# Optimization experiments

Hardware: AMD Instinct MI355X
Metric: run time of the kernel (lower is better)

Reference implementation:

```python
import jax, jax.numpy as jnp
import numpy as np

V, E, H = 32000, 512, 512  # output_dim, emb_dim, hid_dim
B, S = 256, 128


def setup_inputs() -> dict:
    key = jax.random.key(0)
    ks = jax.random.split(key, 16)
    d = {
        'input_ids': jax.random.randint(ks[0], (B,), 0, V),
        'encoded': jax.random.normal(ks[1], (B, S, 2 * H), jnp.float32),
        'src': jax.random.randint(ks[2], (B, S), 0, V),
        'prev_state': jax.random.normal(ks[3], (B, H), jnp.float32),
        'weighted': jax.random.normal(ks[4], (B, 2 * H), jnp.float32),
        'order': 1,
        # parameters (PyTorch layouts: Linear weight is (out,in); GRU gates order r,z,n)
        'embed_w': jax.random.normal(ks[5], (V, E), jnp.float32) * 0.02,
        'gru_w_ih': jax.random.normal(ks[6], (3 * H, E + 2 * H), jnp.float32) * 0.02,
        'gru_w_hh': jax.random.normal(ks[7], (3 * H, H), jnp.float32) * 0.02,
        'gru_b_ih': jnp.zeros((3 * H,), jnp.float32),
        'gru_b_hh': jnp.zeros((3 * H,), jnp.float32),
        'Ws_w': jax.random.normal(ks[8], (H, 2 * H), jnp.float32) * 0.02,
        'Ws_b': jnp.zeros((H,), jnp.float32),
        'Wo_w': jax.random.normal(ks[9], (V, H), jnp.float32) * 0.02,
        'Wo_b': jnp.zeros((V,), jnp.float32),
        'Wc_w': jax.random.normal(ks[10], (H, 2 * H), jnp.float32) * 0.02,
        'Wc_b': jnp.zeros((H,), jnp.float32),
    }
    return d


def _forward(input_ids, encoded, src, prev_state, weighted, order,
             embed_w, gru_w_ih, gru_w_hh, gru_b_ih, gru_b_hh,
             Ws_w, Ws_b, Wo_w, Wo_b, Wc_w, Wc_b):
    b, s, _ = encoded.shape
    v = Wo_w.shape[0]
    if order == 0:
        prev_state = encoded[:, -1] @ Ws_w.T + Ws_b           # (B,H)
        weighted = jnp.zeros((b, 2 * gru_w_hh.shape[1]), encoded.dtype)
    # GRU cell, single step (seq_len=1), torch gate order r,z,n
    x = jnp.concatenate([embed_w[input_ids], weighted], axis=-1)  # (B, E+2H)
    gi = x @ gru_w_ih.T + gru_b_ih
    gh = prev_state @ gru_w_hh.T + gru_b_hh
    i_r, i_z, i_n = jnp.split(gi, 3, axis=-1)
    h_r, h_z, h_n = jnp.split(gh, 3, axis=-1)
    r = jax.nn.sigmoid(i_r + h_r)
    z = jax.nn.sigmoid(i_z + h_z)
    n = jnp.tanh(i_n + r * h_n)
    hidden = (1.0 - z) * n + z * prev_state                    # (B,H)

    score_g = hidden @ Wo_w.T + Wo_b                           # (B,V)
    score_c = jnp.tanh(encoded @ Wc_w.T + Wc_b)                # (B,S,H)
    score_c = jnp.einsum('bsh,bh->bs', score_c, hidden)        # (B,S)
    mask = (src == 0).astype(encoded.dtype) * -1000.0
    score_c = jnp.tanh(score_c + mask)

    probs = jax.nn.softmax(jnp.concatenate([score_g, score_c], axis=1), axis=1)
    prob_g = probs[:, :v]
    prob_c = probs[:, v:]                                      # (B,S)

    # vectorized scatter-add replacing the nested python loops
    rows = jnp.arange(b)[:, None]
    prob_c_to_g = jnp.zeros((b, v), probs.dtype).at[rows, src].add(prob_c)
    predicted = (prob_g + prob_c_to_g)[:, None, :]             # (B,1,V)

    eq = (src == input_ids[:, None]).astype(encoded.dtype)     # (B,S)
    idx = eq / jnp.maximum(eq.sum(axis=1, keepdims=True), 1.0)
    attn = prob_c * idx                                        # (B,S)
    weighted_out = jnp.einsum('bs,bsd->bd', attn, encoded)     # (B,2H)
    return predicted, hidden, weighted_out


def reference(input_ids, encoded, src, prev_state, weighted, order,
              embed_w, gru_w_ih, gru_w_hh, gru_b_ih, gru_b_hh,
              Ws_w, Ws_b, Wo_w, Wo_b, Wc_w, Wc_b):
    return _forward(input_ids, encoded, src, prev_state, weighted, order,
                    embed_w, gru_w_ih, gru_w_hh, gru_b_ih, gru_b_hh,
                    Ws_w, Ws_b, Wo_w, Wo_b, Wc_w, Wc_b)
```

## Files before the change

kernel.cpp:

```cpp
#include <hip/hip_runtime.h>
#include <cstdint>
#include <cstddef>

#define B_ 256
#define S_ 128
#define H_ 512
#define E_ 512
#define V_ 32000
#define NBLK_G (V_ / 64)

typedef _Float16 half_t;
typedef _Float16 half8 __attribute__((ext_vector_type(8)));
typedef float floatx4 __attribute__((ext_vector_type(4)));

__device__ __forceinline__ float sigmoidf_(float x) { return 1.0f / (1.0f + __expf(-x)); }
__device__ __forceinline__ float fast_tanh(float x) {
    float e = __expf(2.0f * x);
    return 1.0f - 2.0f / (e + 1.0f);
}

__global__ __launch_bounds__(256)
void prep_kernel(const int* __restrict__ ids, const float* __restrict__ encoded,
                 const float* __restrict__ prev_state, const float* __restrict__ weighted,
                 const int* __restrict__ order_p, const float* __restrict__ embed,
                 const float* __restrict__ Ws_w, const float* __restrict__ Ws_b,
                 float* __restrict__ x, float* __restrict__ prev)
{
    int i = blockIdx.x * 256 + threadIdx.x;
    int b = i >> 11;
    int j = i & 2047;
    int order = order_p[0];
    if (j < 1536) {
        float v;
        if (j < 512) v = embed[(size_t)ids[b] * E_ + j];
        else         v = (order == 0) ? 0.0f : weighted[b * 1024 + (j - 512)];
        x[b * 1536 + j] = v;
    } else {
        int h = j - 1536;
        float v;
        if (order != 0) {
            v = prev_state[b * H_ + h];
        } else {
            const float* e  = encoded + ((size_t)b * S_ + (S_ - 1)) * 1024;
            const float* wr = Ws_w + (size_t)h * 1024;
            float accv = Ws_b[h];
            for (int k = 0; k < 1024; ++k) accv += e[k] * wr[k];
            v = accv;
        }
        prev[b * H_ + h] = v;
    }
}

__global__ __launch_bounds__(256)
void wc_cvt_kernel(const float* __restrict__ Wc, half_t* __restrict__ out)
{
    int i = blockIdx.x * 256 + threadIdx.x;
    int nc = i & 15;
    int kq = (i >> 4) & 3;
    int kt = (i >> 6) & 31;
    int nt = i >> 11;
    int n  = nt * 16 + nc;
    int k0 = kt * 32 + kq * 8;
    const float* p = Wc + (size_t)n * 1024 + k0;
    float4 a = *(const float4*)p;
    float4 b = *(const float4*)(p + 4);
    half8 h;
    h[0] = (half_t)a.x; h[1] = (half_t)a.y; h[2] = (half_t)a.z; h[3] = (half_t)a.w;
    h[4] = (half_t)b.x; h[5] = (half_t)b.y; h[6] = (half_t)b.z; h[7] = (half_t)b.w;
    *(half8*)(out + (size_t)i * 8) = h;
}

template<int BM, int BN, int WAVES_M, int WAVES_N, int EPI>
__global__ __launch_bounds__(256, 2)
void gemm_f16(const float* __restrict__ A, const float* __restrict__ Bw,
              float* __restrict__ C, const float* __restrict__ bias,
              float* __restrict__ aux, int K, int lda, int ldb, int ldc, int nblk)
{
    constexpr int BK = 32;
    constexpr int WM = BM / WAVES_M;
    constexpr int WN = BN / WAVES_N;
    constexpr int FM = WM / 16;
    constexpr int FN = WN / 16;
    constexpr int A_ITEMS = (BM * 4) / 256;
    constexpr int B_ITEMS = (BN * 4) / 256;

    __shared__ half_t As[BM * BK];
    __shared__ half_t Bs[BN * BK];

    const int tid  = threadIdx.x;
    const int wid  = tid >> 6;
    const int lane = tid & 63;
    const int wm   = wid % WAVES_M;
    const int wn   = wid / WAVES_M;
    const int bm0  = blockIdx.y * BM;
    const int bn0  = blockIdx.x * BN;
    const int col  = lane & 15;
    const int quad = lane >> 4;
    const int swz  = (quad ^ (col & 3)) * 8;

    floatx4 acc[FM][FN] = {};

    for (int kt = 0; kt < K; kt += BK) {
        float4 ar[A_ITEMS][2], br[B_ITEMS][2];
#pragma unroll
        for (int i = 0; i < A_ITEMS; ++i) {
            int idx = tid + i * 256, row = idx >> 2, ch = idx & 3;
            const float* p = A + (size_t)(bm0 + row) * lda + kt + ch * 8;
            ar[i][0] = *(const float4*)p; ar[i][1] = *(const float4*)(p + 4);
        }
#pragma unroll
        for (int i = 0; i < B_ITEMS; ++i) {
            int idx = tid + i * 256, row = idx >> 2, ch = idx & 3;
            const float* p = Bw + (size_t)(bn0 + row) * ldb + kt + ch * 8;
            br[i][0] = *(const float4*)p; br[i][1] = *(const float4*)(p + 4);
        }
        __syncthreads();
#pragma unroll
        for (int i = 0; i < A_ITEMS; ++i) {
            int idx = tid + i * 256, row = idx >> 2, ch = idx & 3;
            int pos = (ch ^ (row & 3)) * 8;
            half8 h;
            h[0] = (half_t)ar[i][0].x; h[1] = (half_t)ar[i][0].y;
            h[2] = (half_t)ar[i][0].z; h[3] = (half_t)ar[i][0].w;
            h[4] = (half_t)ar[i][1].x; h[5] = (half_t)ar[i][1].y;
            h[6] = (half_t)ar[i][1].z; h[7] = (half_t)ar[i][1].w;
            *(half8*)(&As[row * BK + pos]) = h;
        }
#pragma unroll
        for (int i = 0; i < B_ITEMS; ++i) {
            int idx = tid + i * 256, row = idx >> 2, ch = idx & 3;
            int pos = (ch ^ (row & 3)) * 8;
            half8 h;
            h[0] = (half_t)br[i][0].x; h[1] = (half_t)br[i][0].y;
            h[2] = (half_t)br[i][0].z; h[3] = (half_t)br[i][0].w;
            h[4] = (half_t)br[i][1].x; h[5] = (half_t)br[i][1].y;
            h[6] = (half_t)br[i][1].z; h[7] = (half_t)br[i][1].w;
            *(half8*)(&Bs[row * BK + pos]) = h;
        }
        __syncthreads();

        half8 af[FM], bf[FN];
#pragma unroll
        for (int fm = 0; fm < FM; ++fm)
            af[fm] = *(const half8*)(&As[(wm * WM + fm * 16 + col) * BK + swz]);
#pragma unroll
        for (int fn = 0; fn < FN; ++fn)
            bf[fn] = *(const half8*)(&Bs[(wn * WN + fn * 16 + col) * BK + swz]);
#pragma unroll
        for (int fm = 0; fm < FM; ++fm)
#pragma unroll
            for (int fn = 0; fn < FN; ++fn)
                acc[fm][fn] = __builtin_amdgcn_mfma_f32_16x16x32_f16(af[fm], bf[fn], acc[fm][fn], 0, 0, 0);
    }

    if constexpr (EPI == 0) {
#pragma unroll
        for (int fm = 0; fm < FM; ++fm) {
            int m0 = bm0 + wm * WM + fm * 16 + quad * 4;
#pragma unroll
            for (int fn = 0; fn < FN; ++fn) {
                int n = bn0 + wn * WN + fn * 16 + col;
                float bv = bias[n];
#pragma unroll
                for (int r = 0; r < 4; ++r)
                    C[(size_t)(m0 + r) * ldc + n] = acc[fm][fn][r] + bv;
            }
        }
    } else {
        const int bx = blockIdx.x;
#pragma unroll
        for (int fm = 0; fm < FM; ++fm) {
            int m0 = bm0 + wm * WM + fm * 16 + quad * 4;
            float vv[FN][4];
#pragma unroll
            for (int fn = 0; fn < FN; ++fn) {
                int n = bn0 + fn * 16 + col;
                float bv = bias[n];
#pragma unroll
                for (int r = 0; r < 4; ++r) {
                    vv[fn][r] = acc[fm][fn][r] + bv;
                    C[(size_t)(m0 + r) * ldc + n] = vv[fn][r];
                }
            }
#pragma unroll
            for (int r = 0; r < 4; ++r) {
                float mx = vv[0][r];
#pragma unroll
                for (int fn = 1; fn < FN; ++fn) mx = fmaxf(mx, vv[fn][r]);
#pragma unroll
                for (int off = 1; off < 16; off <<= 1)
                    mx = fmaxf(mx, __shfl_xor(mx, off, 64));
                float se = 0.f;
#pragma unroll
                for (int fn = 0; fn < FN; ++fn) se += __expf(vv[fn][r] - mx);
#pragma unroll
                for (int off = 1; off < 16; off <<= 1)
                    se += __shfl_xor(se, off, 64);
                if (col == 0) {
                    aux[(size_t)(m0 + r) * nblk + bx] = mx;
                    aux[(size_t)256 * nblk + (size_t)(m0 + r) * nblk + bx] = se;
                }
            }
        }
    }
}

__global__ __launch_bounds__(512, 4)
void wc_sc_kernel(const float* __restrict__ enc, const half_t* __restrict__ WcT,
                  const float* __restrict__ bias, const float* __restrict__ hidden,
                  float* __restrict__ sc_out)
{
    __shared__ half_t As[2][64 * 32];
    __shared__ float  s_part[8 * 64];

    const int tid  = threadIdx.x;
    const int wid  = tid >> 6;
    const int lane = tid & 63;
    const int col  = lane & 15;
    const int quad = lane >> 4;
    const int swz  = (quad ^ (col & 3)) * 8;
    const int bm0  = blockIdx.x * 64;

    const int ar_row = tid >> 2;
    const int ar_ch  = tid & 3;
    const float* aptr = enc + (size_t)(bm0 + ar_row) * 1024 + ar_ch * 8;
    const int a_pos = ar_row * 32 + (ar_ch ^ (ar_row & 3)) * 8;

    const half_t* bq = WcT + (size_t)wid * 4 * 16384 + quad * 128 + col * 8;

    floatx4 acc[4][4] = {};
    float4 ar0, ar1;
    half8 bf0[4], bf1[4];

    if (tid < 256) { ar0 = *(const float4*)(aptr); ar1 = *(const float4*)(aptr + 4); }
#pragma unroll
    for (int fn = 0; fn < 4; ++fn)
        bf0[fn] = *(const half8*)(bq + fn * 16384);

    for (int t2 = 0; t2 < 16; ++t2) {
        const int kA = t2 * 64;
        if (tid < 256) {
            half8 h;
            h[0] = (half_t)ar0.x; h[1] = (half_t)ar0.y; h[2] = (half_t)ar0.z; h[3] = (half_t)ar0.w;
            h[4] = (half_t)ar1.x; h[5] = (half_t)ar1.y; h[6] = (half_t)ar1.z; h[7] = (half_t)ar1.w;
            *(half8*)(&As[0][a_pos]) = h;
        }
        __syncthreads();
        if (tid < 256) {
            ar0 = *(const float4*)(aptr + kA + 32);
            ar1 = *(const float4*)(aptr + kA + 36);
        }
#pragma unroll
        for (int fn = 0; fn < 4; ++fn)
            bf1[fn] = *(const half8*)(bq + fn * 16384 + (2 * t2 + 1) * 512);
#pragma unroll
        for (int fm = 0; fm < 4; ++fm) {
            half8 af = *(const half8*)(&As[0][(fm * 16 + col) * 32 + swz]);
#pragma unroll
            for (int fn = 0; fn < 4; ++fn)
                acc[fm][fn] = __builtin_amdgcn_mfma_f32_16x16x32_f16(af, bf0[fn], acc[fm][fn], 0, 0, 0);
        }
        if (tid < 256) {
            half8 h;
            h[0] = (half_t)ar0.x; h[1] = (half_t)ar0.y; h[2] = (half_t)ar0.z; h[3] = (half_t)ar0.w;
            h[4] = (half_t)ar1.x; h[5] = (half_t)ar1.y; h[6] = (half_t)ar1.z; h[7] = (half_t)ar1.w;
            *(half8*)(&As[1][a_pos]) = h;
        }
        __syncthreads();
        if (t2 < 15) {
            if (tid < 256) {
                ar0 = *(const float4*)(aptr + kA + 64);
                ar1 = *(const float4*)(aptr + kA + 68);
            }
#pragma unroll
            for (int fn = 0; fn < 4; ++fn)
                bf0[fn] = *(const half8*)(bq + fn * 16384 + (2 * t2 + 2) * 512);
        }
#pragma unroll
        for (int fm = 0; fm < 4; ++fm) {
            half8 af = *(const half8*)(&As[1][(fm * 16 + col) * 32 + swz]);
#pragma unroll
            for (int fn = 0; fn < 4; ++fn)
                acc[fm][fn] = __builtin_amdgcn_mfma_f32_16x16x32_f16(af, bf1[fn], acc[fm][fn], 0, 0, 0);
        }
    }

    const float* hid = hidden + (size_t)(bm0 >> 7) * H_;
#pragma unroll
    for (int fm = 0; fm < 4; ++fm) {
        float p0 = 0.f, p1 = 0.f, p2 = 0.f, p3 = 0.f;
#pragma unroll
        for (int fn = 0; fn < 4; ++fn) {
            int n = wid * 64 + fn * 16 + col;
            float bv = bias[n];
            float hv = hid[n];
            p0 += fast_tanh(acc[fm][fn][0] + bv) * hv;
            p1 += fast_tanh(acc[fm][fn][1] + bv) * hv;
            p2 += fast_tanh(acc[fm][fn][2] + bv) * hv;
            p3 += fast_tanh(acc[fm][fn][3] + bv) * hv;
        }
#pragma unroll
        for (int off = 1; off < 16; off <<= 1) {
            p0 += __shfl_xor(p0, off, 64);
            p1 += __shfl_xor(p1, off, 64);
            p2 += __shfl_xor(p2, off, 64);
            p3 += __shfl_xor(p3, off, 64);
        }
        if (col == 0) {
            int rloc = fm * 16 + quad * 4;
            s_part[wid * 64 + rloc + 0] = p0;
            s_part[wid * 64 + rloc + 1] = p1;
            s_part[wid * 64 + rloc + 2] = p2;
            s_part[wid * 64 + rloc + 3] = p3;
        }
    }
    __syncthreads();
    if (tid < 64) {
        float s = 0.f;
#pragma unroll
        for (int w = 0; w < 8; ++w) s += s_part[w * 64 + tid];
        sc_out[bm0 + tid] = s;
    }
}

__global__ __launch_bounds__(256)
void gate_kernel(const float* __restrict__ gi, const float* __restrict__ gh,
                 const float* __restrict__ prev, float* __restrict__ hidden)
{
    int i = blockIdx.x * 256 + threadIdx.x;
    int b = i >> 9;
    int h = i & 511;
    const float* gib = gi + (size_t)b * 1536;
    const float* ghb = gh + (size_t)b * 1536;
    float r = sigmoidf_(gib[h] + ghb[h]);
    float z = sigmoidf_(gib[h + 512] + ghb[h + 512]);
    float n = tanhf(gib[h + 1024] + r * ghb[h + 1024]);
    hidden[i] = (1.0f - z) * n + z * prev[i];
}

__global__ __launch_bounds__(256)
void final_kernel(const float* __restrict__ sc_raw,
                  const int* __restrict__ src, const int* __restrict__ ids,
                  const float* __restrict__ encoded, const float* __restrict__ parts,
                  float* __restrict__ predicted, float* __restrict__ weighted_out)
{
    int b = blockIdx.x;
    int t = threadIdx.x;
    __shared__ float s_scf[S_];
    __shared__ float s_attn[S_];
    __shared__ int   s_src[S_];
    __shared__ float rm[4], rs[4];
    __shared__ int   s_cnt;

    float* pred = predicted + (size_t)b * V_;
    const float* pm = parts + (size_t)b * NBLK_G;
    const float* ps = parts + (size_t)256 * NBLK_G + (size_t)b * NBLK_G;

    if (t < S_) {
        int sv = src[b * S_ + t];
        s_src[t] = sv;
        float raw = sc_raw[b * S_ + t];
        if (sv == 0) raw -= 1000.0f;
        s_scf[t] = tanhf(raw);
    }

    float m = -1e30f, s = 0.f;
    for (int j = t; j < NBLK_G; j += 256) {
        float mo = pm[j], so = ps[j];
        float mn = fmaxf(m, mo);
        s = s * __expf(m - mn) + so * __expf(mo - mn);
        m = mn;
    }
    __syncthreads();
    if (t < S_) {
        float x = s_scf[t];
        float mn = fmaxf(m, x);
        s = s * __expf(m - mn) + __expf(x - mn);
        m = mn;
    }
#pragma unroll
    for (int off = 1; off < 64; off <<= 1) {
        float mo = __shfl_xor(m, off, 64);
        float so = __shfl_xor(s, off, 64);
        float mn = fmaxf(m, mo);
        s = s * __expf(m - mn) + so * __expf(mo - mn);
        m = mn;
    }
    if ((t & 63) == 0) { rm[t >> 6] = m; rs[t >> 6] = s; }
    __syncthreads();
    float M = rm[0], Z = rs[0];
#pragma unroll
    for (int w = 1; w < 4; ++w) {
        float mo = rm[w], so = rs[w];
        float mn = fmaxf(M, mo);
        Z = Z * __expf(M - mn) + so * __expf(mo - mn);
        M = mn;
    }
    float invZ = 1.0f / Z;

    float4* pr4 = (float4*)pred;
    for (int i = t; i < V_ / 4; i += 256) {
        float4 x = pr4[i];
        float4 o;
        o.x = __expf(x.x - M) * invZ;
        o.y = __expf(x.y - M) * invZ;
        o.z = __expf(x.z - M) * invZ;
        o.w = __expf(x.w - M) * invZ;
        pr4[i] = o;
    }

    int ii = ids[b];
    if (t == 0) {
        int c = 0;
        for (int s2 = 0; s2 < S_; ++s2) c += (s_src[s2] == ii) ? 1 : 0;
        s_cnt = (c > 0) ? c : 1;
    }
    __syncthreads();

    if (t < S_) {
        float pc = __expf(s_scf[t] - M) * invZ;
        atomicAdd(&pred[s_src[t]], pc);
        s_attn[t] = (s_src[t] == ii) ? pc / (float)s_cnt : 0.f;
    }
    __syncthreads();

    const float* eb = encoded + (size_t)b * S_ * 1024;
    for (int d = t; d < 1024; d += 256) {
        float accv = 0.f;
        for (int s2 = 0; s2 < S_; ++s2) {
            float a = s_attn[s2];
            if (a != 0.f) accv += a * eb[s2 * 1024 + d];
        }
        weighted_out[b * 1024 + d] = accv;
    }
}

extern "C" void kernel_launch(void* const* d_in, const int* in_sizes, int n_in,
                              void* d_out, int out_size, void* d_ws, size_t ws_size,
                              hipStream_t stream)
{
    const int*   input_ids  = (const int*)d_in[0];
    const float* encoded    = (const float*)d_in[1];
    const int*   src        = (const int*)d_in[2];
    const float* prev_state = (const float*)d_in[3];
    const float* weighted   = (const float*)d_in[4];
    const int*   order      = (const int*)d_in[5];
    const float* embed_w    = (const float*)d_in[6];
    const float* gru_w_ih   = (const float*)d_in[7];
    const float* gru_w_hh   = (const float*)d_in[8];
    const float* gru_b_ih   = (const float*)d_in[9];
    const float* gru_b_hh   = (const float*)d_in[10];
    const float* Ws_w       = (const float*)d_in[11];
    const float* Ws_b       = (const float*)d_in[12];
    const float* Wo_w       = (const float*)d_in[13];
    const float* Wo_b       = (const float*)d_in[14];
    const float* Wc_w       = (const float*)d_in[15];
    const float* Wc_b       = (const float*)d_in[16];
    (void)in_sizes; (void)n_in; (void)out_size; (void)ws_size;

    float* predicted    = (float*)d_out;
    float* hidden       = predicted + (size_t)B_ * V_;
    float* weighted_out = hidden + (size_t)B_ * H_;

    char* w = (char*)d_ws;
    float* x_f32  = (float*)w;  w += (size_t)B_ * 1536 * 4;
    float* prev_f = (float*)w;  w += (size_t)B_ * H_ * 4;
    float* gi     = (float*)w;  w += (size_t)B_ * 1536 * 4;
    float* gh     = (float*)w;  w += (size_t)B_ * 1536 * 4;
    float* sc_raw = (float*)w;  w += (size_t)B_ * S_ * 4;
    float* parts  = (float*)w;  w += (size_t)2 * B_ * NBLK_G * 4;
    half_t* wc_h  = (half_t*)w; w += (size_t)H_ * 1024 * 2;

    wc_cvt_kernel<<<256, 256, 0, stream>>>(Wc_w, wc_h);

    prep_kernel<<<2048, 256, 0, stream>>>(input_ids, encoded, prev_state, weighted,
                                          order, embed_w, Ws_w, Ws_b, x_f32, prev_f);

    gemm_f16<64, 64, 2, 2, 0><<<dim3(1536 / 64, 256 / 64), 256, 0, stream>>>(
        x_f32, gru_w_ih, gi, gru_b_ih, nullptr, 1536, 1536, 1536, 1536, 0);
    gemm_f16<64, 64, 2, 2, 0><<<dim3(1536 / 64, 256 / 64), 256, 0, stream>>>(
        prev_f, gru_w_hh, gh, gru_b_hh, nullptr, 512, 512, 512, 1536, 0);

    gate_kernel<<<(B_ * H_) / 256, 256, 0, stream>>>(gi, gh, prev_f, hidden);

    wc_sc_kernel<<<(B_ * S_) / 64, 512, 0, stream>>>(encoded, wc_h, Wc_b, hidden, sc_raw);

    gemm_f16<256, 64, 4, 1, 2><<<dim3(NBLK_G, 1), 256, 0, stream>>>(
        hidden, Wo_w, predicted, Wo_b, parts, 512, 512, 512, V_, NBLK_G);

    final_kernel<<<B_, 256, 0, stream>>>(sc_raw, src, input_ids, encoded, parts,
                                         predicted, weighted_out);
}
```

Before: 450.2 us.

## Merge launches, restructure Wc score GEMM, widen final kernel blocks

Folds the Wc fp32-to-fp16 conversion into the prep kernel as extra blocks, and merges the two GRU GEMMs into one gru_gemm launch that selects its operands by block index. This removes two kernel launches. The wc_sc kernel now loads 64-wide K tiles with all 512 threads, uses XOR-swizzled double-buffered LDS with one barrier per phase, and raises wave priority around the MFMA block. The final kernel moves to 1024 threads per block to spread the softmax normalisation and the weighted sum over more threads, at the cost of a larger block-level reduction.

Result: faster. 414.9 us (-7.8%).

```diff
diff --git a/kernel.cpp b/kernel.cpp
--- a/kernel.cpp
+++ b/kernel.cpp
@@ -24,8 +24,24 @@
                  const float* __restrict__ prev_state, const float* __restrict__ weighted,
                  const int* __restrict__ order_p, const float* __restrict__ embed,
                  const float* __restrict__ Ws_w, const float* __restrict__ Ws_b,
-                 float* __restrict__ x, float* __restrict__ prev)
-{
+                 float* __restrict__ x, float* __restrict__ prev,
+                 const float* __restrict__ Wc, half_t* __restrict__ wc_out)
+{
+    if (blockIdx.x >= 2048) {
+        int i = (blockIdx.x - 2048) * 256 + threadIdx.x;
+        int nc = i & 15;
+        int kq = (i >> 4) & 3;
+        int kt = (i >> 6) & 31;
+        int nt = i >> 11;
+        const float* p = Wc + (size_t)(nt * 16 + nc) * 1024 + kt * 32 + kq * 8;
+        float4 a = *(const float4*)p;
+        float4 b = *(const float4*)(p + 4);
+        half8 h;
+        h[0] = (half_t)a.x; h[1] = (half_t)a.y; h[2] = (half_t)a.z; h[3] = (half_t)a.w;
+        h[4] = (half_t)b.x; h[5] = (half_t)b.y; h[6] = (half_t)b.z; h[7] = (half_t)b.w;
+        *(half8*)(wc_out + (size_t)i * 8) = h;
+        return;
+    }
     int i = blockIdx.x * 256 + threadIdx.x;
     int b = i >> 11;
     int j = i & 2047;
@@ -51,25 +67,6 @@
     }
 }
 
-__global__ __launch_bounds__(256)
-void wc_cvt_kernel(const float* __restrict__ Wc, half_t* __restrict__ out)
-{
-    int i = blockIdx.x * 256 + threadIdx.x;
-    int nc = i & 15;
-    int kq = (i >> 4) & 3;
-    int kt = (i >> 6) & 31;
-    int nt = i >> 11;
-    int n  = nt * 16 + nc;
-    int k0 = kt * 32 + kq * 8;
-    const float* p = Wc + (size_t)n * 1024 + k0;
-    float4 a = *(const float4*)p;
-    float4 b = *(const float4*)(p + 4);
-    half8 h;
-    h[0] = (half_t)a.x; h[1] = (half_t)a.y; h[2] = (half_t)a.z; h[3] = (half_t)a.w;
-    h[4] = (half_t)b.x; h[5] = (half_t)b.y; h[6] = (half_t)b.z; h[7] = (half_t)b.w;
-    *(half8*)(out + (size_t)i * 8) = h;
-}
-
 template<int BM, int BN, int WAVES_M, int WAVES_N, int EPI>
 __global__ __launch_bounds__(256, 2)
 void gemm_f16(const float* __restrict__ A, const float* __restrict__ Bw,
@@ -205,12 +202,89 @@
     }
 }
 
+__global__ __launch_bounds__(256, 2)
+void gru_gemm(const float* __restrict__ x, const float* __restrict__ prevf,
+              const float* __restrict__ Wih, const float* __restrict__ Whh,
+              const float* __restrict__ bih, const float* __restrict__ bhh,
+              float* __restrict__ gi, float* __restrict__ gh)
+{
+    constexpr int BK = 32;
+    __shared__ half_t As[64 * BK];
+    __shared__ half_t Bs[64 * BK];
+
+    const int sel = (blockIdx.x >= 24) ? 1 : 0;
+    const float* A    = sel ? prevf : x;
+    const float* Bw   = sel ? Whh : Wih;
+    float*       C    = sel ? gh : gi;
+    const float* bias = sel ? bhh : bih;
+    const int K   = sel ? 512 : 1536;
+    const int lda = sel ? 512 : 1536;
+    const int ldb = lda;
+    const int bn0 = (sel ? blockIdx.x - 24 : blockIdx.x) * 64;
+    const int bm0 = blockIdx.y * 64;
+
+    const int tid  = threadIdx.x;
+    const int wid  = tid >> 6;
+    const int lane = tid & 63;
+    const int wm   = wid & 1;
+    const int wn   = wid >> 1;
+    const int col  = lane & 15;
+    const int quad = lane >> 4;
+    const int swz  = (quad ^ (col & 3)) * 8;
+
+    floatx4 acc[2][2] = {};
+
+    for (int kt = 0; kt < K; kt += BK) {
+        int row = tid >> 2, ch = tid & 3;
+        const float* pa = A + (size_t)(bm0 + row) * lda + kt + ch * 8;
+        const float* pb = Bw + (size_t)(bn0 + row) * ldb + kt + ch * 8;
+        float4 a0 = *(const float4*)pa, a1 = *(const float4*)(pa + 4);
+        float4 b0 = *(const float4*)pb, b1 = *(const float4*)(pb + 4);
+        __syncthreads();
+        int pos = row * BK + (ch ^ (row & 3)) * 8;
+        half8 ha, hb;
+        ha[0] = (half_t)a0.x; ha[1] = (half_t)a0.y; ha[2] = (half_t)a0.z; ha[3] = (half_t)a0.w;
+        ha[4] = (half_t)a1.x; ha[5] = (half_t)a1.y; ha[6] = (half_t)a1.z; ha[7] = (half_t)a1.w;
+        hb[0] = (half_t)b0.x; hb[1] = (half_t)b0.y; hb[2] = (half_t)b0.z; hb[3] = (half_t)b0.w;
+        hb[4] = (half_t)b1.x; hb[5] = (half_t)b1.y; hb[6] = (half_t)b1.z; hb[7] = (half_t)b1.w;
+        *(half8*)(&As[pos]) = ha;
+        *(half8*)(&Bs[pos]) = hb;
+        __syncthreads();
+
+        half8 af[2], bf[2];
+#pragma unroll
+        for (int fm = 0; fm < 2; ++fm)
+            af[fm] = *(const half8*)(&As[(wm * 32 + fm * 16 + col) * BK + swz]);
+#pragma unroll
+        for (int fn = 0; fn < 2; ++fn)
+            bf[fn] = *(const half8*)(&Bs[(wn * 32 + fn * 16 + col) * BK + swz]);
+#pragma unroll
+        for (int fm = 0; fm < 2; ++fm)
+#pragma unroll
+            for (int fn = 0; fn < 2; ++fn)
+                acc[fm][fn] = __builtin_amdgcn_mfma_f32_16x16x32_f16(af[fm], bf[fn], acc[fm][fn], 0, 0, 0);
+    }
+
+#pragma unroll
+    for (int fm = 0; fm < 2; ++fm) {
+        int m0 = bm0 + wm * 32 + fm * 16 + quad * 4;
+#pragma unroll
+        for (int fn = 0; fn < 2; ++fn) {
+            int n = bn0 + wn * 32 + fn * 16 + col;
+            float bv = bias[n];
+#pragma unroll
+            for (int r = 0; r < 4; ++r)
+                C[(size_t)(m0 + r) * 1536 + n] = acc[fm][fn][r] + bv;
+        }
+    }
+}
+
 __global__ __launch_bounds__(512, 4)
 void wc_sc_kernel(const float* __restrict__ enc, const half_t* __restrict__ WcT,
                   const float* __restrict__ bias, const float* __restrict__ hidden,
                   float* __restrict__ sc_out)
 {
-    __shared__ half_t As[2][64 * 32];
+    __shared__ half_t As[2][64 * 64];
     __shared__ float  s_part[8 * 64];
 
     const int tid  = threadIdx.x;
@@ -218,71 +292,54 @@
     const int lane = tid & 63;
     const int col  = lane & 15;
     const int quad = lane >> 4;
-    const int swz  = (quad ^ (col & 3)) * 8;
     const int bm0  = blockIdx.x * 64;
 
-    const int ar_row = tid >> 2;
-    const int ar_ch  = tid & 3;
+    const int ar_row = tid >> 3;
+    const int ar_ch  = tid & 7;
     const float* aptr = enc + (size_t)(bm0 + ar_row) * 1024 + ar_ch * 8;
-    const int a_pos = ar_row * 32 + (ar_ch ^ (ar_row & 3)) * 8;
-
-    const half_t* bq = WcT + (size_t)wid * 4 * 16384 + quad * 128 + col * 8;
+    const int a_pos = ar_row * 64 + ((ar_ch ^ (ar_row & 7)) * 8);
+
+    const half_t* bq = WcT + (size_t)wid * 65536 + quad * 128 + col * 8;
 
     floatx4 acc[4][4] = {};
     float4 ar0, ar1;
-    half8 bf0[4], bf1[4];
-
-    if (tid < 256) { ar0 = *(const float4*)(aptr); ar1 = *(const float4*)(aptr + 4); }
-#pragma unroll
-    for (int fn = 0; fn < 4; ++fn)
-        bf0[fn] = *(const half8*)(bq + fn * 16384);
-
-    for (int t2 = 0; t2 < 16; ++t2) {
-        const int kA = t2 * 64;
-        if (tid < 256) {
+
+    ar0 = *(const float4*)(aptr);
+    ar1 = *(const float4*)(aptr + 4);
+
+    for (int ph = 0; ph < 16; ++ph) {
+        const int buf = ph & 1;
+        {
             half8 h;
             h[0] = (half_t)ar0.x; h[1] = (half_t)ar0.y; h[2] = (half_t)ar0.z; h[3] = (half_t)ar0.w;
             h[4] = (half_t)ar1.x; h[5] = (half_t)ar1.y; h[6] = (half_t)ar1.z; h[7] = (half_t)ar1.w;
-            *(half8*)(&As[0][a_pos]) = h;
+            *(half8*)(&As[buf][a_pos]) = h;
         }
         __syncthreads();
-        if (tid < 256) {
-            ar0 = *(const float4*)(aptr + kA + 32);
-            ar1 = *(const float4*)(aptr + kA + 36);
-        }
-#pragma unroll
-        for (int fn = 0; fn < 4; ++fn)
-            bf1[fn] = *(const half8*)(bq + fn * 16384 + (2 * t2 + 1) * 512);
+        if (ph < 15) {
+            ar0 = *(const float4*)(aptr + (ph + 1) * 64);
+            ar1 = *(const float4*)(aptr + (ph + 1) * 64 + 4);
+        }
+        half8 bf[2][4];
+#pragma unroll
+        for (int j = 0; j < 2; ++j)
+#pragma unroll
+            for (int fn = 0; fn < 4; ++fn)
+                bf[j][fn] = *(const half8*)(bq + (size_t)fn * 16384 + (2 * ph + j) * 512);
+
+        __builtin_amdgcn_s_setprio(1);
 #pragma unroll
         for (int fm = 0; fm < 4; ++fm) {
-            half8 af = *(const half8*)(&As[0][(fm * 16 + col) * 32 + swz]);
-#pragma unroll
-            for (int fn = 0; fn < 4; ++fn)
-                acc[fm][fn] = __builtin_amdgcn_mfma_f32_16x16x32_f16(af, bf0[fn], acc[fm][fn], 0, 0, 0);
-        }
-        if (tid < 256) {
-            half8 h;
-            h[0] = (half_t)ar0.x; h[1] = (half_t)ar0.y; h[2] = (half_t)ar0.z; h[3] = (half_t)ar0.w;
-            h[4] = (half_t)ar1.x; h[5] = (half_t)ar1.y; h[6] = (half_t)ar1.z; h[7] = (half_t)ar1.w;
-            *(half8*)(&As[1][a_pos]) = h;
-        }
-        __syncthreads();
-        if (t2 < 15) {
-            if (tid < 256) {
-                ar0 = *(const float4*)(aptr + kA + 64);
-                ar1 = *(const float4*)(aptr + kA + 68);
+            const int row = fm * 16 + col;
+#pragma unroll
+            for (int j = 0; j < 2; ++j) {
+                half8 af = *(const half8*)(&As[buf][row * 64 + (((j * 4 + quad) ^ (row & 7)) * 8)]);
+#pragma unroll
+                for (int fn = 0; fn < 4; ++fn)
+                    acc[fm][fn] = __builtin_amdgcn_mfma_f32_16x16x32_f16(af, bf[j][fn], acc[fm][fn], 0, 0, 0);
             }
-#pragma unroll
-            for (int fn = 0; fn < 4; ++fn)
-                bf0[fn] = *(const half8*)(bq + fn * 16384 + (2 * t2 + 2) * 512);
-        }
-#pragma unroll
-        for (int fm = 0; fm < 4; ++fm) {
-            half8 af = *(const half8*)(&As[1][(fm * 16 + col) * 32 + swz]);
-#pragma unroll
-            for (int fn = 0; fn < 4; ++fn)
-                acc[fm][fn] = __builtin_amdgcn_mfma_f32_16x16x32_f16(af, bf1[fn], acc[fm][fn], 0, 0, 0);
-        }
+        }
+        __builtin_amdgcn_s_setprio(0);
     }
 
     const float* hid = hidden + (size_t)(bm0 >> 7) * H_;
@@ -338,7 +395,7 @@
     hidden[i] = (1.0f - z) * n + z * prev[i];
 }
 
-__global__ __launch_bounds__(256)
+__global__ __launch_bounds__(1024)
 void final_kernel(const float* __restrict__ sc_raw,
                   const int* __restrict__ src, const int* __restrict__ ids,
                   const float* __restrict__ encoded, const float* __restrict__ parts,
@@ -349,7 +406,7 @@
     __shared__ float s_scf[S_];
     __shared__ float s_attn[S_];
     __shared__ int   s_src[S_];
-    __shared__ float rm[4], rs[4];
+    __shared__ float rm[16], rs[16];
     __shared__ int   s_cnt;
 
     float* pred = predicted + (size_t)b * V_;
@@ -365,7 +422,7 @@
     }
 
     float m = -1e30f, s = 0.f;
-    for (int j = t; j < NBLK_G; j += 256) {
+    for (int j = t; j < NBLK_G; j += 1024) {
         float mo = pm[j], so = ps[j];
         float mn = fmaxf(m, mo);
         s = s * __expf(m - mn) + so * __expf(mo - mn);
@@ -390,7 +447,7 @@
     __syncthreads();
     float M = rm[0], Z = rs[0];
 #pragma unroll
-    for (int w = 1; w < 4; ++w) {
+    for (int w = 1; w < 16; ++w) {
         float mo = rm[w], so = rs[w];
         float mn = fmaxf(M, mo);
         Z = Z * __expf(M - mn) + so * __expf(mo - mn);
@@ -399,7 +456,7 @@
     float invZ = 1.0f / Z;
 
     float4* pr4 = (float4*)pred;
-    for (int i = t; i < V_ / 4; i += 256) {
+    for (int i = t; i < V_ / 4; i += 1024) {
         float4 x = pr4[i];
         float4 o;
         o.x = __expf(x.x - M) * invZ;
@@ -425,7 +482,7 @@
     __syncthreads();
 
     const float* eb = encoded + (size_t)b * S_ * 1024;
-    for (int d = t; d < 1024; d += 256) {
+    for (int d = t; d < 1024; d += 1024) {
         float accv = 0.f;
         for (int s2 = 0; s2 < S_; ++s2) {
             float a = s_attn[s2];
@@ -471,15 +528,12 @@
     float* parts  = (float*)w;  w += (size_t)2 * B_ * NBLK_G * 4;
     half_t* wc_h  = (half_t*)w; w += (size_t)H_ * 1024 * 2;
 
-    wc_cvt_kernel<<<256, 256, 0, stream>>>(Wc_w, wc_h);
-
-    prep_kernel<<<2048, 256, 0, stream>>>(input_ids, encoded, prev_state, weighted,
-                                          order, embed_w, Ws_w, Ws_b, x_f32, prev_f);
-
-    gemm_f16<64, 64, 2, 2, 0><<<dim3(1536 / 64, 256 / 64), 256, 0, stream>>>(
-        x_f32, gru_w_ih, gi, gru_b_ih, nullptr, 1536, 1536, 1536, 1536, 0);
-    gemm_f16<64, 64, 2, 2, 0><<<dim3(1536 / 64, 256 / 64), 256, 0, stream>>>(
-        prev_f, gru_w_hh, gh, gru_b_hh, nullptr, 512, 512, 512, 1536, 0);
+    prep_kernel<<<2304, 256, 0, stream>>>(input_ids, encoded, prev_state, weighted,
+                                          order, embed_w, Ws_w, Ws_b, x_f32, prev_f,
+                                          Wc_w, wc_h);
+
+    gru_gemm<<<dim3(48, 4), 256, 0, stream>>>(x_f32, prev_f, gru_w_ih, gru_w_hh,
+                                              gru_b_ih, gru_b_hh, gi, gh);
 
     gate_kernel<<<(B_ * H_) / 256, 256, 0, stream>>>(gi, gh, prev_f, hidden);
 
@@ -488,6 +542,6 @@
     gemm_f16<256, 64, 4, 1, 2><<<dim3(NBLK_G, 1), 256, 0, stream>>>(
         hidden, Wo_w, predicted, Wo_b, parts, 512, 512, 512, V_, NBLK_G);
 
-    final_kernel<<<B_, 256, 0, stream>>>(sc_raw, src, input_ids, encoded, parts,
-                                         predicted, weighted_out);
-}
+    final_kernel<<<B_, 1024, 0, stream>>>(sc_raw, src, input_ids, encoded, parts,
+                                          predicted, weighted_out);
+}
```
